# Optimization experiments

Measured on AMD Instinct MI355X. Metric: run time of the kernel, lower is better.

Reference implementation:

```python
import jax, jax.numpy as jnp
import numpy as np

H = 16   # num_heads
K = 2    # top_k experts per token


def _layer_norm(x, g, b, eps=1e-5):
    mu = jnp.mean(x, axis=-1, keepdims=True)
    var = jnp.mean(jnp.square(x - mu), axis=-1, keepdims=True)
    return (x - mu) * jax.lax.rsqrt(var + eps) * g + b


def setup_inputs() -> dict:
    key = jax.random.key(0)
    ks = jax.random.split(key, 8)
    B, S, D, E = 2, 2048, 1024, 8
    sc = 0.02
    return {
        "x": jax.random.normal(ks[0], (B, S, D), jnp.float32),
        "wq": jax.random.normal(ks[1], (D, D), jnp.float32) * sc,
        "wk": jax.random.normal(ks[2], (D, D), jnp.float32) * sc,
        "wv": jax.random.normal(ks[3], (D, D), jnp.float32) * sc,
        "wo": jax.random.normal(ks[4], (D, D), jnp.float32) * sc,
        "ln1_g": jnp.ones((D,), jnp.float32),
        "ln1_b": jnp.zeros((D,), jnp.float32),
        "ln2_g": jnp.ones((D,), jnp.float32),
        "ln2_b": jnp.zeros((D,), jnp.float32),
        "router_w": jax.random.normal(ks[5], (E, D), jnp.float32) * sc,
        "expert_w": jax.random.normal(ks[6], (E, D, D), jnp.float32) * sc,
    }


def reference(x, wq, wk, wv, wo, ln1_g, ln1_b, ln2_g, ln2_b, router_w, expert_w):
    B, S, D = x.shape
    E = expert_w.shape[0]
    hd = D // H

    # ---- attention sublayer: x = x + attn(norm1(x)) ----
    h = _layer_norm(x, ln1_g, ln1_b)
    q = (h @ wq.T).reshape(B, S, H, hd).transpose(0, 2, 1, 3)  # bhsd
    k = (h @ wk.T).reshape(B, S, H, hd).transpose(0, 2, 1, 3)
    v = (h @ wv.T).reshape(B, S, H, hd).transpose(0, 2, 1, 3)
    scores = jnp.einsum("bhqd,bhkd->bhqk", q, k) / jnp.sqrt(jnp.float32(hd))
    causal = jnp.tril(jnp.ones((S, S), dtype=bool))
    scores = jnp.where(causal, scores, jnp.finfo(scores.dtype).min)
    probs = jax.nn.softmax(scores, axis=-1)
    attn = jnp.einsum("bhqk,bhkd->bhqd", probs, v)
    attn = attn.transpose(0, 2, 1, 3).reshape(B, S, D) @ wo.T
    x = x + attn

    # ---- MoE sublayer: x = x + moe(norm2(x)) ----
    h2 = _layer_norm(x, ln2_g, ln2_b)
    logits = jnp.einsum("bsd,ed->bse", h2, router_w)          # [B,S,E]
    top_logits, top_ids = jax.lax.top_k(logits, K)            # [B,S,K]
    gates = jax.nn.softmax(top_logits, axis=-1)               # [B,S,K]
    # dense combine weights over experts (E is small): sum_k gate_k * onehot(id_k)
    combine = jnp.sum(jax.nn.one_hot(top_ids, E, dtype=h2.dtype) * gates[..., None], axis=-2)  # [B,S,E]
    # per-token matvec with expert weights: token @ W_e.T for each expert, then weighted sum
    y = jnp.einsum("bsd,eod->bseo", h2, expert_w)             # [B,S,E,D]
    moe_out = jnp.einsum("bse,bseo->bso", combine, y)
    return x + moe_out
```

## Files before the change

kernel.cpp:

```cpp
#include <hip/hip_runtime.h>
#include <hip/hip_bf16.h>
#include <cstdint>


typedef __bf16 bf16;
typedef __bf16 bf16x8 __attribute__((ext_vector_type(8)));
typedef __bf16 bf16x4 __attribute__((ext_vector_type(4)));
typedef float f32x4 __attribute__((ext_vector_type(4)));
typedef float f32x16 __attribute__((ext_vector_type(16)));

#define MFMA(a, b, c) __builtin_amdgcn_mfma_f32_16x16x32_bf16(a, b, c, 0, 0, 0)
#define MFMA32(a, b, c) __builtin_amdgcn_mfma_f32_32x32x16_bf16(a, b, c, 0, 0, 0)

__device__ __forceinline__ void gld16(void* lds, const void* g) {
  __builtin_amdgcn_global_load_lds(
      (const __attribute__((address_space(1))) void*)g,
      (__attribute__((address_space(3))) void*)lds, 16, 0, 0);
}

__global__ void prep_weights(const float* __restrict__ wq, const float* __restrict__ wk,
                             const float* __restrict__ wv, const float* __restrict__ wo,
                             const float* __restrict__ expw,
                             bf16* __restrict__ wqh, bf16* __restrict__ wql,
                             bf16* __restrict__ wkh, bf16* __restrict__ wkl,
                             bf16* __restrict__ wvh, bf16* __restrict__ wvl,
                             bf16* __restrict__ woh, bf16* __restrict__ wol,
                             bf16* __restrict__ ewh) {
  int bid = blockIdx.x;
  if (bid < 4096) {
    int wsel = bid >> 10;
    const float* src = wsel == 0 ? wq : wsel == 1 ? wk : wsel == 2 ? wv : wo;
    bf16* hi = wsel == 0 ? wqh : wsel == 1 ? wkh : wsel == 2 ? wvh : woh;
    bf16* lo = wsel == 0 ? wql : wsel == 1 ? wkl : wsel == 2 ? wvl : wol;
    int i = ((bid & 1023) * 256 + threadIdx.x) * 4;
    float4 v = *(const float4*)(src + i);
    float a[4] = {v.x, v.y, v.z, v.w};
#pragma unroll
    for (int j = 0; j < 4; j++) {
      bf16 h = (bf16)a[j];
      hi[i + j] = h;
      lo[i + j] = (bf16)(a[j] - (float)h);
    }
  } else {
    int i = ((bid - 4096) * 256 + threadIdx.x) * 4;
    float4 v = *(const float4*)(expw + i);
    ewh[i] = (bf16)v.x; ewh[i + 1] = (bf16)v.y;
    ewh[i + 2] = (bf16)v.z; ewh[i + 3] = (bf16)v.w;
  }
}

__global__ void ln_split(const float* __restrict__ x, const float* __restrict__ g,
                         const float* __restrict__ b, bf16* __restrict__ hi,
                         bf16* __restrict__ lo) {
  int tok = blockIdx.x, t = threadIdx.x;
  float4 v = ((const float4*)(x + (size_t)tok * 1024))[t];
  float s = v.x + v.y + v.z + v.w;
  float ss = v.x * v.x + v.y * v.y + v.z * v.z + v.w * v.w;
#pragma unroll
  for (int o = 1; o < 64; o <<= 1) { s += __shfl_xor(s, o); ss += __shfl_xor(ss, o); }
  __shared__ float red[8];
  int w = t >> 6, lane = t & 63;
  if (lane == 0) { red[w] = s; red[4 + w] = ss; }
  __syncthreads();
  s = red[0] + red[1] + red[2] + red[3];
  ss = red[4] + red[5] + red[6] + red[7];
  float mu = s * (1.f / 1024.f);
  float rstd = rsqrtf(ss * (1.f / 1024.f) - mu * mu + 1e-5f);
  float4 gv = ((const float4*)g)[t], bv = ((const float4*)b)[t];
  float y[4] = {(v.x - mu) * rstd * gv.x + bv.x, (v.y - mu) * rstd * gv.y + bv.y,
                (v.z - mu) * rstd * gv.z + bv.z, (v.w - mu) * rstd * gv.w + bv.w};
  size_t o = (size_t)tok * 1024 + t * 4;
#pragma unroll
  for (int j = 0; j < 4; j++) {
    bf16 h = (bf16)y[j];
    hi[o + j] = h;
    lo[o + j] = (bf16)(y[j] - (float)h);
  }
}

__global__ void ln2route(const float* __restrict__ x1, const float* __restrict__ g,
                         const float* __restrict__ b, const float* __restrict__ rw,
                         bf16* __restrict__ h2h, int* __restrict__ eid,
                         float2* __restrict__ gout) {
  int tok = blockIdx.x, t = threadIdx.x;
  float4 v = ((const float4*)(x1 + (size_t)tok * 1024))[t];
  float s = v.x + v.y + v.z + v.w;
  float ss = v.x * v.x + v.y * v.y + v.z * v.z + v.w * v.w;
#pragma unroll
  for (int o = 1; o < 64; o <<= 1) { s += __shfl_xor(s, o); ss += __shfl_xor(ss, o); }
  __shared__ float red[8];
  __shared__ float h2s[1024];
  __shared__ float lg[8];
  int w = t >> 6, lane = t & 63;
  if (lane == 0) { red[w] = s; red[4 + w] = ss; }
  __syncthreads();
  s = red[0] + red[1] + red[2] + red[3];
  ss = red[4] + red[5] + red[6] + red[7];
  float mu = s * (1.f / 1024.f);
  float rstd = rsqrtf(ss * (1.f / 1024.f) - mu * mu + 1e-5f);
  float4 gv = ((const float4*)g)[t], bv = ((const float4*)b)[t];
  float4 y;
  y.x = (v.x - mu) * rstd * gv.x + bv.x;
  y.y = (v.y - mu) * rstd * gv.y + bv.y;
  y.z = (v.z - mu) * rstd * gv.z + bv.z;
  y.w = (v.w - mu) * rstd * gv.w + bv.w;
  ((float4*)h2s)[t] = y;
  size_t o = (size_t)tok * 1024 + t * 4;
  h2h[o] = (bf16)y.x; h2h[o + 1] = (bf16)y.y;
  h2h[o + 2] = (bf16)y.z; h2h[o + 3] = (bf16)y.w;
  __syncthreads();
  float a0 = 0.f, a1 = 0.f;
  const float4* r0 = (const float4*)(rw + (2 * w) * 1024);
  const float4* r1 = (const float4*)(rw + (2 * w + 1) * 1024);
#pragma unroll
  for (int it = 0; it < 4; it++) {
    float4 xv = ((const float4*)h2s)[lane + 64 * it];
    float4 w0 = r0[lane + 64 * it];
    float4 w1 = r1[lane + 64 * it];
    a0 += xv.x * w0.x + xv.y * w0.y + xv.z * w0.z + xv.w * w0.w;
    a1 += xv.x * w1.x + xv.y * w1.y + xv.z * w1.z + xv.w * w1.w;
  }
#pragma unroll
  for (int o2 = 1; o2 < 64; o2 <<= 1) {
    a0 += __shfl_xor(a0, o2);
    a1 += __shfl_xor(a1, o2);
  }
  if (lane == 0) { lg[2 * w] = a0; lg[2 * w + 1] = a1; }
  __syncthreads();
  if (t == 0) {
    int i0 = 0; float l0 = lg[0];
#pragma unroll
    for (int e = 1; e < 8; e++) if (lg[e] > l0) { l0 = lg[e]; i0 = e; }
    int i1 = -1; float l1 = -3e38f;
#pragma unroll
    for (int e = 0; e < 8; e++) if (e != i0 && lg[e] > l1) { l1 = lg[e]; i1 = e; }
    float e1 = __expf(l1 - l0);
    float den = 1.f + e1;
    eid[tok] = i0 | (i1 << 4);
    gout[tok] = make_float2(1.f / den, e1 / den);
  }
}

__global__ void build_lists(const int* __restrict__ eid,
                            const float2* __restrict__ gv,
                            int* __restrict__ tlist, float* __restrict__ glist,
                            int* __restrict__ cnt) {
  int e = blockIdx.x, t = threadIdx.x;
  int lane = t & 63, w = t >> 6;
  __shared__ int wt[4];
  int base = 0;
  for (int c = 0; c < 16; c++) {
    int tok = c * 256 + t;
    int pair = eid[tok];
    int e0 = pair & 15, e1 = pair >> 4;
    bool p = (e0 == e) || (e1 == e);
    float2 g2 = gv[tok];
    float gate = (e0 == e) ? g2.x : g2.y;
    unsigned long long m = __ballot(p);
    int rank = __popcll(m & ((1ull << lane) - 1ull));
    if (lane == 0) wt[w] = __popcll(m);
    __syncthreads();
    int off = base;
    for (int i = 0; i < w; i++) off += wt[i];
    if (p) {
      tlist[e * 4096 + off + rank] = tok;
      glist[e * 4096 + off + rank] = gate;
    }
    base += wt[0] + wt[1] + wt[2] + wt[3];
    __syncthreads();
  }
  if (t == 0) cnt[e] = base;
  int pad = (base + 127) & ~127;
  if (pad > 4096) pad = 4096;
  for (int i = base + t; i < pad; i += 256) {
    tlist[e * 4096 + i] = 0;
    glist[e * 4096 + i] = 0.f;
  }
}

__device__ __forceinline__ void gemm_core_split(
    const bf16* __restrict__ Ah, const bf16* __restrict__ Al,
    const bf16* __restrict__ Bh, const bf16* __restrict__ Bl, int m0, int n0,
    f32x4 (&acc)[4][4]) {
  __shared__ __align__(16) bf16 As_h[4096], As_l[4096], Bs_h[4096], Bs_l[4096];
  int t = threadIdx.x, lane = t & 63, w = t >> 6;
  int i0 = t, i1 = t + 256;
  const bf16* a0h = Ah + (size_t)(m0 + (i0 >> 2)) * 1024 + (i0 & 3) * 8;
  const bf16* a1h = Ah + (size_t)(m0 + (i1 >> 2)) * 1024 + (i1 & 3) * 8;
  const bf16* a0l = Al + (size_t)(m0 + (i0 >> 2)) * 1024 + (i0 & 3) * 8;
  const bf16* a1l = Al + (size_t)(m0 + (i1 >> 2)) * 1024 + (i1 & 3) * 8;
  const bf16* b0h = Bh + (size_t)(n0 + (i0 >> 2)) * 1024 + (i0 & 3) * 8;
  const bf16* b1h = Bh + (size_t)(n0 + (i1 >> 2)) * 1024 + (i1 & 3) * 8;
  const bf16* b0l = Bl + (size_t)(n0 + (i0 >> 2)) * 1024 + (i0 & 3) * 8;
  const bf16* b1l = Bl + (size_t)(n0 + (i1 >> 2)) * 1024 + (i1 & 3) * 8;
  int wm = (w >> 1) * 64, wn = (w & 1) * 64;
  int lr = lane & 15, lq = lane >> 4;
  for (int k0 = 0; k0 < 1024; k0 += 32) {
    __syncthreads();
    gld16(&As_h[i0 * 8], a0h + k0); gld16(&As_h[i1 * 8], a1h + k0);
    gld16(&As_l[i0 * 8], a0l + k0); gld16(&As_l[i1 * 8], a1l + k0);
    gld16(&Bs_h[i0 * 8], b0h + k0); gld16(&Bs_h[i1 * 8], b1h + k0);
    gld16(&Bs_l[i0 * 8], b0l + k0); gld16(&Bs_l[i1 * 8], b1l + k0);
    __syncthreads();
    bf16x8 ah[4], al4[4], bh[4], bl4[4];
#pragma unroll
    for (int i = 0; i < 4; i++) {
      ah[i]  = *(const bf16x8*)&As_h[(wm + i * 16 + lr) * 32 + lq * 8];
      al4[i] = *(const bf16x8*)&As_l[(wm + i * 16 + lr) * 32 + lq * 8];
      bh[i]  = *(const bf16x8*)&Bs_h[(wn + i * 16 + lr) * 32 + lq * 8];
      bl4[i] = *(const bf16x8*)&Bs_l[(wn + i * 16 + lr) * 32 + lq * 8];
    }
#pragma unroll
    for (int i = 0; i < 4; i++)
#pragma unroll
      for (int j = 0; j < 4; j++) {
        f32x4 c = acc[i][j];
        c = MFMA(ah[i], bh[j], c);
        c = MFMA(ah[i], bl4[j], c);
        c = MFMA(al4[i], bh[j], c);
        acc[i][j] = c;
      }
  }
}

__global__ __launch_bounds__(256, 2) void gemm_qk(
    const bf16* __restrict__ hh, const bf16* __restrict__ hl,
    const bf16* __restrict__ wqh, const bf16* __restrict__ wql,
    const bf16* __restrict__ wkh, const bf16* __restrict__ wkl,
    bf16* __restrict__ qh, bf16* __restrict__ ql, bf16* __restrict__ kh,
    bf16* __restrict__ kl) {
  int n0 = blockIdx.x * 128, m0 = blockIdx.y * 128, z = blockIdx.z;
  const bf16* Bh = z ? wkh : wqh;
  const bf16* Bl = z ? wkl : wql;
  f32x4 acc[4][4];
#pragma unroll
  for (int i = 0; i < 4; i++)
#pragma unroll
    for (int j = 0; j < 4; j++) acc[i][j] = (f32x4){0.f, 0.f, 0.f, 0.f};
  gemm_core_split(hh, hl, Bh, Bl, m0, n0, acc);
  int t = threadIdx.x, lane = t & 63, w = t >> 6;
  int wm = (w >> 1) * 64, wn = (w & 1) * 64, lr = lane & 15, lq = lane >> 4;
  bf16* Oh = z ? kh : qh;
  bf16* Ol = z ? kl : ql;
  float scale = z ? 1.0f : (0.125f * 1.44269504f);
#pragma unroll
  for (int i = 0; i < 4; i++)
#pragma unroll
    for (int j = 0; j < 4; j++)
#pragma unroll
      for (int r = 0; r < 4; r++) {
        size_t row = m0 + wm + i * 16 + lq * 4 + r;
        int col = n0 + wn + j * 16 + lr;
        float v = acc[i][j][r] * scale;
        bf16 h = (bf16)v;
        Oh[row * 1024 + col] = h;
        Ol[row * 1024 + col] = (bf16)(v - (float)h);
      }
}

__global__ __launch_bounds__(256, 2) void gemm_v(
    const bf16* __restrict__ A, const bf16* __restrict__ B,
    bf16* __restrict__ vth) {
  int n0 = blockIdx.x * 128, m0 = blockIdx.y * 128;
  __shared__ __align__(16) bf16 As[4096], Bs[4096];
  int t = threadIdx.x, lane = t & 63, w = t >> 6;
  int i0 = t, i1 = t + 256;
  const bf16* a0 = A + (size_t)(m0 + (i0 >> 2)) * 1024 + (i0 & 3) * 8;
  const bf16* a1 = A + (size_t)(m0 + (i1 >> 2)) * 1024 + (i1 & 3) * 8;
  const bf16* b0 = B + (size_t)(n0 + (i0 >> 2)) * 1024 + (i0 & 3) * 8;
  const bf16* b1 = B + (size_t)(n0 + (i1 >> 2)) * 1024 + (i1 & 3) * 8;
  int wm = (w >> 1) * 64, wn = (w & 1) * 64, lr = lane & 15, lq = lane >> 4;
  f32x4 acc[4][4];
#pragma unroll
  for (int i = 0; i < 4; i++)
#pragma unroll
    for (int j = 0; j < 4; j++) acc[i][j] = (f32x4){0.f, 0.f, 0.f, 0.f};
  for (int k0 = 0; k0 < 1024; k0 += 32) {
    __syncthreads();
    gld16(&As[i0 * 8], a0 + k0); gld16(&As[i1 * 8], a1 + k0);
    gld16(&Bs[i0 * 8], b0 + k0); gld16(&Bs[i1 * 8], b1 + k0);
    __syncthreads();
    bf16x8 af[4], bfr[4];
#pragma unroll
    for (int i = 0; i < 4; i++) {
      af[i] = *(const bf16x8*)&As[(wm + i * 16 + lr) * 32 + lq * 8];
      bfr[i] = *(const bf16x8*)&Bs[(wn + i * 16 + lr) * 32 + lq * 8];
    }
#pragma unroll
    for (int i = 0; i < 4; i++)
#pragma unroll
      for (int j = 0; j < 4; j++) acc[i][j] = MFMA(af[i], bfr[j], acc[i][j]);
  }
  int bb = m0 >> 11;
  int srow0 = m0 & 2047;
#pragma unroll
  for (int i = 0; i < 4; i++)
#pragma unroll
    for (int j = 0; j < 4; j++) {
      int col = n0 + wn + j * 16 + lr;
      int head = col >> 6, d = col & 63;
      int s = srow0 + wm + i * 16 + lq * 4;
      int ss = (s & ~63) | (((((s >> 2) & 15)) ^ (d & 15)) << 2);
      bf16x4 hv;
#pragma unroll
      for (int r = 0; r < 4; r++) hv[r] = (bf16)acc[i][j][r];
      size_t off = ((size_t)((bb * 16 + head) * 64 + d)) * 2048 + ss;
      *(bf16x4*)(vth + off) = hv;
    }
}

__global__ __launch_bounds__(256, 2) void gemm_wo(
    const bf16* __restrict__ ah, const bf16* __restrict__ al,
    const bf16* __restrict__ bh, const bf16* __restrict__ bl,
    const float* __restrict__ resid, float* __restrict__ outp) {
  int n0 = blockIdx.x * 128, m0 = blockIdx.y * 128;
  f32x4 acc[4][4];
#pragma unroll
  for (int i = 0; i < 4; i++)
#pragma unroll
    for (int j = 0; j < 4; j++) acc[i][j] = (f32x4){0.f, 0.f, 0.f, 0.f};
  gemm_core_split(ah, al, bh, bl, m0, n0, acc);
  int t = threadIdx.x, lane = t & 63, w = t >> 6;
  int wm = (w >> 1) * 64, wn = (w & 1) * 64, lr = lane & 15, lq = lane >> 4;
#pragma unroll
  for (int i = 0; i < 4; i++)
#pragma unroll
    for (int j = 0; j < 4; j++)
#pragma unroll
      for (int r = 0; r < 4; r++) {
        size_t row = m0 + wm + i * 16 + lq * 4 + r;
        int col = n0 + wn + j * 16 + lr;
        outp[row * 1024 + col] = resid[row * 1024 + col] + acc[i][j][r];
      }
}

__global__ __launch_bounds__(256, 2) void attn_fused(
    const bf16* __restrict__ qh, const bf16* __restrict__ ql,
    const bf16* __restrict__ kh, const bf16* __restrict__ kl,
    const bf16* __restrict__ vth,
    bf16* __restrict__ oh, bf16* __restrict__ ol) {
  const int S = 2048, D = 1024;
  int qt = 15 - blockIdx.y;
  int hb = blockIdx.x;
  int head = hb & 15, b = hb >> 4;
  int qb = qt * 128;
  int t = threadIdx.x, lane = t & 63, w = t >> 6;
  int l31 = lane & 31, l5 = lane >> 5;
  int base = b * S, hcol = head * 64;

  __shared__ __align__(16) bf16 Kh_s[2][4096], Kl_s[2][4096];
  __shared__ __align__(16) bf16 Vh_s[2][4096];
  __shared__ float Ls[128];

  bf16x8 qfh[4], qfl[4];
  {
    const bf16* p1 = qh + (size_t)(base + qb + w * 32 + l31) * D + hcol + l5 * 8;
    const bf16* p2 = ql + (size_t)(base + qb + w * 32 + l31) * D + hcol + l5 * 8;
#pragma unroll
    for (int c = 0; c < 4; c++) {
      qfh[c] = *(const bf16x8*)(p1 + 16 * c);
      qfl[c] = *(const bf16x8*)(p2 + 16 * c);
    }
  }
  f32x16 O0, O1;
  float lsum = 0.f;
#pragma unroll
  for (int r = 0; r < 16; r++) { O0[r] = 0.f; O1[r] = 0.f; }

  int r0 = t >> 3, p0 = t & 7;
  int g0 = p0 ^ (r0 & 7);
  const bf16* k0hp = kh + (size_t)(base + r0) * D + hcol + g0 * 8;
  const bf16* k1hp = kh + (size_t)(base + 32 + r0) * D + hcol + g0 * 8;
  const bf16* k0lp = kl + (size_t)(base + r0) * D + hcol + g0 * 8;
  const bf16* k1lp = kl + (size_t)(base + 32 + r0) * D + hcol + g0 * 8;
  const bf16* v0hp = vth + (size_t)(hb * 64 + r0) * 2048 + p0 * 8;
  const bf16* v1hp = vth + (size_t)(hb * 64 + 32 + r0) * 2048 + p0 * 8;

  int qwmin = qb + w * 32;
  int nt = 2 * qt + 2;

#define STAGE(kts, bb) do { \
    gld16(&Kh_s[bb][t * 8], k0hp + (size_t)(kts) * D); \
    gld16(&Kh_s[bb][2048 + t * 8], k1hp + (size_t)(kts) * D); \
    gld16(&Kl_s[bb][t * 8], k0lp + (size_t)(kts) * D); \
    gld16(&Kl_s[bb][2048 + t * 8], k1lp + (size_t)(kts) * D); \
    gld16(&Vh_s[bb][t * 8], v0hp + (kts)); \
    gld16(&Vh_s[bb][2048 + t * 8], v1hp + (kts)); \
  } while (0)

  STAGE(0, 0);
  __syncthreads();

  for (int ti = 0; ti < nt; ti++) {
    int kt = ti * 64;
    int bb = ti & 1;
    if (ti + 1 < nt) STAGE((ti + 1) * 64, bb ^ 1);
    if (kt <= qwmin + 31) {
      bool skip1 = (kt + 32 > qwmin + 31);
#pragma unroll
      for (int ktile = 0; ktile < 2; ktile++) {
        if (ktile == 1 && skip1) break;
        bool maskt = (kt + 32 * ktile + 31 > qwmin);
        int keyr = ktile * 32 + l31;
        f32x16 scA, scB;
#pragma unroll
        for (int r = 0; r < 16; r++) { scA[r] = 0.f; scB[r] = 0.f; }
        __builtin_amdgcn_s_setprio(1);
#pragma unroll
        for (int c = 0; c < 4; c++) {
          int dg = ((2 * c + l5) ^ (keyr & 7)) * 8;
          bf16x8 kv = *(const bf16x8*)&Kh_s[bb][keyr * 64 + dg];
          bf16x8 km = *(const bf16x8*)&Kl_s[bb][keyr * 64 + dg];
          if (c < 2) {
            scA = MFMA32(kv, qfh[c], scA);
            scA = MFMA32(kv, qfl[c], scA);
            scA = MFMA32(km, qfh[c], scA);
          } else {
            scB = MFMA32(kv, qfh[c], scB);
            scB = MFMA32(kv, qfl[c], scB);
            scB = MFMA32(km, qfh[c], scB);
          }
        }
        __builtin_amdgcn_s_setprio(0);
        int kb0 = kt + 32 * ktile + 4 * l5;
        int qg = qwmin + l31;
        float pvv[16];
#pragma unroll
        for (int r = 0; r < 16; r++) {
          int cst = (r & 3) + 8 * (r >> 2);
          float sv = scA[r] + scB[r];
          if (maskt && (kb0 + cst > qg)) sv = -30000.f;
          float p = __builtin_amdgcn_exp2f(sv);
          pvv[r] = p;
          lsum += p;
        }
        uint32_t hw[4][2], lw[4][2];
#pragma unroll
        for (int o = 0; o < 4; o++)
#pragma unroll
          for (int j = 0; j < 2; j++) {
            int ra = 4 * o + 2 * j;
            bf16 h0 = (bf16)pvv[ra], h1 = (bf16)pvv[ra + 1];
            union { bf16 h[2]; uint32_t u; } ph, pl;
            ph.h[0] = h0; ph.h[1] = h1;
            pl.h[0] = (bf16)(pvv[ra] - (float)h0);
            pl.h[1] = (bf16)(pvv[ra + 1] - (float)h1);
            hw[o][j] = ph.u;
            lw[o][j] = pl.u;
          }
#pragma unroll
        for (int c2 = 0; c2 < 2; c2++) {
          union { uint32_t u[4]; bf16x8 v; } pa, plo;
          pa.u[0] = hw[2 * c2][0];     pa.u[1] = hw[2 * c2][1];
          pa.u[2] = hw[2 * c2 + 1][0]; pa.u[3] = hw[2 * c2 + 1][1];
          plo.u[0] = lw[2 * c2][0];     plo.u[1] = lw[2 * c2][1];
          plo.u[2] = lw[2 * c2 + 1][0]; plo.u[3] = lw[2 * c2 + 1][1];
          __builtin_amdgcn_s_setprio(1);
#pragma unroll
          for (int dtile = 0; dtile < 2; dtile++) {
            int d = dtile * 32 + l31;
            int pqA = ((8 * ktile + 4 * c2 + l5) ^ (d & 15)) * 4;
            union { bf16x4 q[2]; bf16x8 v; } vbu;
            vbu.q[0] = *(const bf16x4*)&Vh_s[bb][d * 64 + pqA];
            vbu.q[1] = *(const bf16x4*)&Vh_s[bb][d * 64 + (pqA ^ 8)];
            if (dtile == 0) {
              O0 = MFMA32(pa.v, vbu.v, O0);
              O0 = MFMA32(plo.v, vbu.v, O0);
            } else {
              O1 = MFMA32(pa.v, vbu.v, O1);
              O1 = MFMA32(plo.v, vbu.v, O1);
            }
          }
          __builtin_amdgcn_s_setprio(0);
        }
      }
    }
    __syncthreads();
  }
#undef STAGE
  float ltot = lsum + __shfl_xor(lsum, 32);
  if (lane < 32) Ls[w * 32 + l31] = ltot;
#pragma unroll
  for (int r = 0; r < 16; r++) {
    int qlocal = (r & 3) + 8 * (r >> 2) + 4 * l5;
    float linv = 1.f / Ls[w * 32 + qlocal];
    size_t tok = (size_t)(base + qb + w * 32 + qlocal);
    float v0 = O0[r] * linv;
    float v1 = O1[r] * linv;
    bf16 h0 = (bf16)v0, h1 = (bf16)v1;
    oh[tok * D + hcol + l31] = h0;
    ol[tok * D + hcol + l31] = (bf16)(v0 - (float)h0);
    oh[tok * D + hcol + 32 + l31] = h1;
    ol[tok * D + hcol + 32 + l31] = (bf16)(v1 - (float)h1);
  }
}

__global__ __launch_bounds__(256, 2) void gemm_moe(
    const bf16* __restrict__ A, const bf16* __restrict__ W,
    const int* __restrict__ tlist, const float* __restrict__ glist,
    const int* __restrict__ cnt, float* __restrict__ outp) {
  int e = blockIdx.z;
  int count = cnt[e];
  int m0 = blockIdx.y * 128;
  if (m0 >= count) return;
  int n0 = blockIdx.x * 128;
  const int* tl = tlist + e * 4096;
  const bf16* B = W + (size_t)e * 1024 * 1024;
  __shared__ __align__(16) bf16 As[4096], Bs[4096];
  int t = threadIdx.x, lane = t & 63, w = t >> 6;
  int i0 = t, i1 = t + 256;
  int ra = tl[m0 + (i0 >> 2)], rb = tl[m0 + (i1 >> 2)];
  const bf16* a0 = A + (size_t)ra * 1024 + (i0 & 3) * 8;
  const bf16* a1 = A + (size_t)rb * 1024 + (i1 & 3) * 8;
  const bf16* b0 = B + (size_t)(n0 + (i0 >> 2)) * 1024 + (i0 & 3) * 8;
  const bf16* b1 = B + (size_t)(n0 + (i1 >> 2)) * 1024 + (i1 & 3) * 8;
  int wm = (w >> 1) * 64, wn = (w & 1) * 64, lr = lane & 15, lq = lane >> 4;
  f32x4 acc[4][4];
#pragma unroll
  for (int i = 0; i < 4; i++)
#pragma unroll
    for (int j = 0; j < 4; j++) acc[i][j] = (f32x4){0.f, 0.f, 0.f, 0.f};
  for (int k0 = 0; k0 < 1024; k0 += 32) {
    __syncthreads();
    gld16(&As[i0 * 8], a0 + k0); gld16(&As[i1 * 8], a1 + k0);
    gld16(&Bs[i0 * 8], b0 + k0); gld16(&Bs[i1 * 8], b1 + k0);
    __syncthreads();
    bf16x8 af[4], bfr[4];
#pragma unroll
    for (int i = 0; i < 4; i++) {
      af[i] = *(const bf16x8*)&As[(wm + i * 16 + lr) * 32 + lq * 8];
      bfr[i] = *(const bf16x8*)&Bs[(wn + i * 16 + lr) * 32 + lq * 8];
    }
#pragma unroll
    for (int i = 0; i < 4; i++)
#pragma unroll
      for (int j = 0; j < 4; j++) acc[i][j] = MFMA(af[i], bfr[j], acc[i][j]);
  }
#pragma unroll
  for (int i = 0; i < 4; i++)
#pragma unroll
    for (int r = 0; r < 4; r++) {
      int slot = m0 + wm + i * 16 + lq * 4 + r;
      if (slot < count) {
        int tok = tl[slot];
        float gte = glist[e * 4096 + slot];
#pragma unroll
        for (int j = 0; j < 4; j++) {
          int col = n0 + wn + j * 16 + lr;
          atomicAdd(&outp[(size_t)tok * 1024 + col], gte * acc[i][j][r]);
        }
      }
    }
}

extern "C" void kernel_launch(void* const* d_in, const int* in_sizes, int n_in,
                              void* d_out, int out_size, void* d_ws, size_t ws_size,
                              hipStream_t stream) {
  (void)in_sizes; (void)n_in; (void)out_size; (void)ws_size;
  const float* x    = (const float*)d_in[0];
  const float* wq   = (const float*)d_in[1];
  const float* wk   = (const float*)d_in[2];
  const float* wv   = (const float*)d_in[3];
  const float* wo   = (const float*)d_in[4];
  const float* ln1g = (const float*)d_in[5];
  const float* ln1b = (const float*)d_in[6];
  const float* ln2g = (const float*)d_in[7];
  const float* ln2b = (const float*)d_in[8];
  const float* rw   = (const float*)d_in[9];
  const float* expw = (const float*)d_in[10];
  float* out = (float*)d_out;

  char* p = (char*)d_ws;
  auto take = [&](size_t bytes) -> char* {
    char* r = p;
    p += (bytes + 255) & ~(size_t)255;
    return r;
  };
  const size_t ND2 = 4096ull * 1024 * 2;
  const size_t WD2 = 1024ull * 1024 * 2;
  bf16* h_hi = (bf16*)take(ND2); bf16* h_lo = (bf16*)take(ND2);
  bf16* wqh = (bf16*)take(WD2); bf16* wql = (bf16*)take(WD2);
  bf16* wkh = (bf16*)take(WD2); bf16* wkl = (bf16*)take(WD2);
  bf16* wvh = (bf16*)take(WD2); bf16* wvl = (bf16*)take(WD2);
  bf16* woh = (bf16*)take(WD2); bf16* wol = (bf16*)take(WD2);
  bf16* q_hi = (bf16*)take(ND2); bf16* q_lo = (bf16*)take(ND2);
  bf16* k_hi = (bf16*)take(ND2); bf16* k_lo = (bf16*)take(ND2);
  bf16* vt_hi = (bf16*)take(ND2);
  bf16* a_hi = (bf16*)take(ND2); bf16* a_lo = (bf16*)take(ND2);
  bf16* h2h  = (bf16*)take(ND2);
  bf16* ewh  = (bf16*)take(8ull * 1024 * 1024 * 2);
  int*   tlist  = (int*)take(8ull * 4096 * 4);
  float* glist  = (float*)take(8ull * 4096 * 4);
  int*   cnt    = (int*)take(64);
  int*   reid   = (int*)take(4096 * 4);
  float2* rg    = (float2*)take(4096 * 8);

  prep_weights<<<12288, 256, 0, stream>>>(wq, wk, wv, wo, expw, wqh, wql, wkh,
                                          wkl, wvh, wvl, woh, wol, ewh);
  ln_split<<<4096, 256, 0, stream>>>(x, ln1g, ln1b, h_hi, h_lo);
  gemm_qk<<<dim3(8, 32, 2), 256, 0, stream>>>(h_hi, h_lo, wqh, wql, wkh, wkl,
                                              q_hi, q_lo, k_hi, k_lo);
  gemm_v<<<dim3(8, 32), 256, 0, stream>>>(h_hi, wvh, vt_hi);
  attn_fused<<<dim3(32, 16), 256, 0, stream>>>(q_hi, q_lo, k_hi, k_lo, vt_hi,
                                               a_hi, a_lo);
  gemm_wo<<<dim3(8, 32), 256, 0, stream>>>(a_hi, a_lo, woh, wol, x, out);
  ln2route<<<4096, 256, 0, stream>>>(out, ln2g, ln2b, rw, h2h, reid, rg);
  build_lists<<<8, 256, 0, stream>>>(reid, rg, tlist, glist, cnt);
  gemm_moe<<<dim3(8, 32, 8), 256, 0, stream>>>(h2h, ewh, tlist, glist, cnt,
                                               out);
}
```

Measured before the change: 418.1 us.

## Split causal attention KV range across blocks with atomic accumulation and finalize kernel

Each (batch, head) attention job is split into 40 blocks. A static table assigns each block a query tile and a KV tile range of at most about 8 tiles, which evens out the causal-mask imbalance and raises the block count. Partial unnormalized outputs and row sums are combined with float atomicAdd into global accumulators. A new attn_final kernel then normalizes and does the hi/lo bf16 split. This adds two memsets, 16MB of atomic traffic and an extra launch, and the occupancy hint is raised to 3 blocks per SM.

New measurement: 418.9 us. No clear change (+0.2%).

```diff
diff --git a/kernel.cpp b/kernel.cpp
--- a/kernel.cpp
+++ b/kernel.cpp
@@ -334,13 +334,27 @@
       }
 }
 
-__global__ __launch_bounds__(256, 2) void attn_fused(
+__global__ __launch_bounds__(256, 3) void attn_fused(
     const bf16* __restrict__ qh, const bf16* __restrict__ ql,
     const bf16* __restrict__ kh, const bf16* __restrict__ kl,
     const bf16* __restrict__ vth,
-    bf16* __restrict__ oh, bf16* __restrict__ ol) {
+    float* __restrict__ O_acc, float* __restrict__ L_acc) {
   const int S = 2048, D = 1024;
-  int qt = 15 - blockIdx.y;
+  static const unsigned char QTt[40] = {
+      15, 15, 15, 15, 14, 14, 14, 13, 13, 13, 12, 12, 12, 11, 11, 11,
+      10, 10, 9, 9, 8, 8, 7, 7, 6, 5, 4, 3,
+      14, 10, 6, 2, 13, 9, 5, 1, 12, 8, 4, 0};
+  static const unsigned char C0t[40] = {
+      0, 8, 16, 24, 0, 8, 16, 0, 8, 16, 0, 8, 16, 0, 8, 16,
+      0, 8, 0, 8, 0, 8, 0, 8, 0, 0, 0, 0,
+      24, 16, 8, 0, 24, 16, 8, 0, 24, 16, 8, 0};
+  static const unsigned char C1t[40] = {
+      8, 16, 24, 32, 8, 16, 24, 8, 16, 24, 8, 16, 24, 8, 16, 24,
+      8, 16, 8, 16, 8, 16, 8, 16, 8, 8, 8, 8,
+      30, 22, 14, 6, 28, 20, 12, 4, 26, 18, 10, 2};
+  int y = blockIdx.y;
+  int qt = QTt[y];
+  int tile0 = C0t[y], tile1 = C1t[y];
   int hb = blockIdx.x;
   int head = hb & 15, b = hb >> 4;
   int qb = qt * 128;
@@ -350,7 +364,6 @@
 
   __shared__ __align__(16) bf16 Kh_s[2][4096], Kl_s[2][4096];
   __shared__ __align__(16) bf16 Vh_s[2][4096];
-  __shared__ float Ls[128];
 
   bf16x8 qfh[4], qfl[4];
   {
@@ -377,7 +390,6 @@
   const bf16* v1hp = vth + (size_t)(hb * 64 + 32 + r0) * 2048 + p0 * 8;
 
   int qwmin = qb + w * 32;
-  int nt = 2 * qt + 2;
 
 #define STAGE(kts, bb) do { \
     gld16(&Kh_s[bb][t * 8], k0hp + (size_t)(kts) * D); \
@@ -388,13 +400,13 @@
     gld16(&Vh_s[bb][2048 + t * 8], v1hp + (kts)); \
   } while (0)
 
-  STAGE(0, 0);
+  STAGE(tile0 * 64, tile0 & 1);
   __syncthreads();
 
-  for (int ti = 0; ti < nt; ti++) {
+  for (int ti = tile0; ti < tile1; ++ti) {
     int kt = ti * 64;
     int bb = ti & 1;
-    if (ti + 1 < nt) STAGE((ti + 1) * 64, bb ^ 1);
+    if (ti + 1 < tile1) STAGE((ti + 1) * 64, bb ^ 1);
     if (kt <= qwmin + 31) {
       bool skip1 = (kt + 32 > qwmin + 31);
 #pragma unroll
@@ -478,21 +490,39 @@
     __syncthreads();
   }
 #undef STAGE
-  float ltot = lsum + __shfl_xor(lsum, 32);
-  if (lane < 32) Ls[w * 32 + l31] = ltot;
-#pragma unroll
-  for (int r = 0; r < 16; r++) {
-    int qlocal = (r & 3) + 8 * (r >> 2) + 4 * l5;
-    float linv = 1.f / Ls[w * 32 + qlocal];
-    size_t tok = (size_t)(base + qb + w * 32 + qlocal);
-    float v0 = O0[r] * linv;
-    float v1 = O1[r] * linv;
-    bf16 h0 = (bf16)v0, h1 = (bf16)v1;
-    oh[tok * D + hcol + l31] = h0;
-    ol[tok * D + hcol + l31] = (bf16)(v0 - (float)h0);
-    oh[tok * D + hcol + 32 + l31] = h1;
-    ol[tok * D + hcol + 32 + l31] = (bf16)(v1 - (float)h1);
-  }
+  if (tile0 * 64 <= qwmin + 31) {
+    float ltot = lsum + __shfl_xor(lsum, 32);
+    if (l5 == 0) {
+      size_t tokq = (size_t)(base + qb + w * 32 + l31);
+      atomicAdd(&L_acc[tokq * 16 + head], ltot);
+    }
+#pragma unroll
+    for (int r = 0; r < 16; r++) {
+      int qlocal = (r & 3) + 8 * (r >> 2) + 4 * l5;
+      size_t tok = (size_t)(base + qb + w * 32 + qlocal);
+      atomicAdd(&O_acc[tok * 1024 + hcol + l31], O0[r]);
+      atomicAdd(&O_acc[tok * 1024 + hcol + 32 + l31], O1[r]);
+    }
+  }
+}
+
+__global__ void attn_final(const float* __restrict__ O_acc,
+                           const float* __restrict__ L_acc,
+                           bf16* __restrict__ oh, bf16* __restrict__ ol) {
+  int tok = blockIdx.x, t = threadIdx.x;
+  float4 v = ((const float4*)(O_acc + (size_t)tok * 1024))[t];
+  float linv = 1.f / L_acc[tok * 16 + (t >> 4)];
+  float a[4] = {v.x * linv, v.y * linv, v.z * linv, v.w * linv};
+  bf16x4 hv, lv;
+#pragma unroll
+  for (int j = 0; j < 4; j++) {
+    bf16 h = (bf16)a[j];
+    hv[j] = h;
+    lv[j] = (bf16)(a[j] - (float)h);
+  }
+  size_t o = (size_t)tok * 1024 + t * 4;
+  *(bf16x4*)(oh + o) = hv;
+  *(bf16x4*)(ol + o) = lv;
 }
 
 __global__ __launch_bounds__(256, 2) void gemm_moe(
@@ -594,15 +624,20 @@
   int*   cnt    = (int*)take(64);
   int*   reid   = (int*)take(4096 * 4);
   float2* rg    = (float2*)take(4096 * 8);
-
+  float* O_acc  = (float*)take(4096ull * 1024 * 4);
+  float* L_acc  = (float*)take(4096ull * 16 * 4);
+
+  hipMemsetAsync(O_acc, 0, 4096ull * 1024 * 4, stream);
+  hipMemsetAsync(L_acc, 0, 4096ull * 16 * 4, stream);
   prep_weights<<<12288, 256, 0, stream>>>(wq, wk, wv, wo, expw, wqh, wql, wkh,
                                           wkl, wvh, wvl, woh, wol, ewh);
   ln_split<<<4096, 256, 0, stream>>>(x, ln1g, ln1b, h_hi, h_lo);
   gemm_qk<<<dim3(8, 32, 2), 256, 0, stream>>>(h_hi, h_lo, wqh, wql, wkh, wkl,
                                               q_hi, q_lo, k_hi, k_lo);
   gemm_v<<<dim3(8, 32), 256, 0, stream>>>(h_hi, wvh, vt_hi);
-  attn_fused<<<dim3(32, 16), 256, 0, stream>>>(q_hi, q_lo, k_hi, k_lo, vt_hi,
-                                               a_hi, a_lo);
+  attn_fused<<<dim3(32, 40), 256, 0, stream>>>(q_hi, q_lo, k_hi, k_lo, vt_hi,
+                                               O_acc, L_acc);
+  attn_final<<<4096, 256, 0, stream>>>(O_acc, L_acc, a_hi, a_lo);
   gemm_wo<<<dim3(8, 32), 256, 0, stream>>>(a_hi, a_lo, woh, wol, x, out);
   ln2route<<<4096, 256, 0, stream>>>(out, ln2g, ln2b, rw, h2h, reid, rg);
   build_lists<<<8, 256, 0, stream>>>(reid, rg, tlist, glist, cnt);
```
